# Optimization experiments

Measured on AMD Instinct MI355X. Metric: run time of the kernel, lower is better.

## Reference

```python
import jax, jax.numpy as jnp
import numpy as np

D_MODEL = 1024
NUM_HEADS = 16
HEAD_DIM = D_MODEL // NUM_HEADS
THETA = 10000.0


def _rope(x, cos, sin):
    # x: [B, H, S, hd]; cos/sin: [S, hd//2] (broadcast over B, H)
    x_even = x[..., 0::2]
    x_odd = x[..., 1::2]
    y_even = x_even * cos - x_odd * sin
    y_odd = x_even * sin + x_odd * cos
    # interleave back: stack on last dim then flatten
    y = jnp.stack((y_even, y_odd), axis=-1)
    return y.reshape(x.shape)


def setup_inputs() -> dict:
    key = jax.random.key(0)
    ks = jax.random.split(key, 5)
    B, S = 2, 2048
    x = jax.random.normal(ks[0], (B, S, D_MODEL), dtype=jnp.float32)
    scale = 1.0 / np.sqrt(D_MODEL)
    Wq = jax.random.normal(ks[1], (D_MODEL, D_MODEL), dtype=jnp.float32) * scale
    Wk = jax.random.normal(ks[2], (D_MODEL, D_MODEL), dtype=jnp.float32) * scale
    Wv = jax.random.normal(ks[3], (D_MODEL, D_MODEL), dtype=jnp.float32) * scale
    Wo = jax.random.normal(ks[4], (D_MODEL, D_MODEL), dtype=jnp.float32) * scale
    token_positions = jnp.arange(S, dtype=jnp.int64 if jax.config.jax_enable_x64 else jnp.int32)
    return {"x": x, "token_positions": token_positions, "Wq": Wq, "Wk": Wk, "Wv": Wv, "Wo": Wo}


def reference(x, token_positions, Wq, Wk, Wv, Wo):
    B, S, _ = x.shape
    # nn.Linear(d,d,bias=False): y = x @ W.T
    q = (x @ Wq.T).reshape(B, S, NUM_HEADS, HEAD_DIM).transpose(0, 2, 1, 3)
    k = (x @ Wk.T).reshape(B, S, NUM_HEADS, HEAD_DIM).transpose(0, 2, 1, 3)
    v = (x @ Wv.T).reshape(B, S, NUM_HEADS, HEAD_DIM).transpose(0, 2, 1, 3)

    # RoPE tables gathered at token_positions
    freqs = 1.0 / THETA ** (jnp.arange(0, HEAD_DIM, 2, dtype=jnp.float32) / HEAD_DIM)
    angles = token_positions.astype(jnp.float32)[:, None] * freqs[None, :]  # [S, hd//2]
    cos, sin = jnp.cos(angles), jnp.sin(angles)
    q = _rope(q, cos, sin)
    k = _rope(k, cos, sin)

    scores = jnp.einsum("bhqd,bhkd->bhqk", q, k) / np.sqrt(HEAD_DIM)
    causal = jnp.tril(jnp.ones((S, S), dtype=bool))
    scores = jnp.where(causal, scores, jnp.finfo(scores.dtype).min)
    attn = jax.nn.softmax(scores, axis=-1)
    out = jnp.einsum("bhqk,bhkd->bhqd", attn, v)  # [B,H,S,hd]
    out = out.transpose(0, 2, 1, 3).reshape(B, S, D_MODEL)
    return out @ Wo.T
```

## Files before the change

### kernel.cpp

```cpp
#include <hip/hip_runtime.h>

#define S_LEN 2048
#define NH 16
#define HD 64
#define DM 1024
#define MTOT 4096

#define QSCALE 0.18033688011112042f

typedef short bf16x8 __attribute__((ext_vector_type(8)));
typedef float f32x4 __attribute__((ext_vector_type(4)));
typedef unsigned short u16x8 __attribute__((ext_vector_type(8)));

__device__ __forceinline__ unsigned short f2bf(float f) {
  unsigned int u = __builtin_bit_cast(unsigned int, f);
  u += 0x7fffu + ((u >> 16) & 1u);
  return (unsigned short)(u >> 16);
}
__device__ __forceinline__ unsigned short f2bf_fast(float f) {
  unsigned int u = __builtin_bit_cast(unsigned int, f);
  return (unsigned short)((u + 0x8000u) >> 16);
}

__device__ __forceinline__ void async_copy16(const void* g, void* l) {
  __builtin_amdgcn_global_load_lds(
      (const __attribute__((address_space(1))) unsigned int*)g,
      (__attribute__((address_space(3))) unsigned int*)l, 16, 0, 0);
}

__global__ void cvt_bf16_kernel(const float* __restrict__ src,
                                unsigned short* __restrict__ dst, int n) {
  int i = (blockIdx.x * 256 + threadIdx.x) * 8;
  if (i >= n) return;
  const float4* s = (const float4*)(src + i);
  float4 v0 = s[0], v1 = s[1];
  u16x8 o;
  o[0] = f2bf(v0.x); o[1] = f2bf(v0.y); o[2] = f2bf(v0.z); o[3] = f2bf(v0.w);
  o[4] = f2bf(v1.x); o[5] = f2bf(v1.y); o[6] = f2bf(v1.z); o[7] = f2bf(v1.w);
  *(u16x8*)(dst + i) = o;
}

__global__ void cvt_w_kernel(const float* __restrict__ w0, const float* __restrict__ w1,
                             const float* __restrict__ w2, const float* __restrict__ w3,
                             unsigned short* __restrict__ dst) {
  int z = blockIdx.y;
  const float* src = (z == 0) ? w0 : (z == 1) ? w1 : (z == 2) ? w2 : w3;
  int i = (blockIdx.x * 256 + threadIdx.x) * 8;
  const float4* s = (const float4*)(src + i);
  float4 v0 = s[0], v1 = s[1];
  u16x8 o;
  o[0] = f2bf(v0.x); o[1] = f2bf(v0.y); o[2] = f2bf(v0.z); o[3] = f2bf(v0.w);
  o[4] = f2bf(v1.x); o[5] = f2bf(v1.y); o[6] = f2bf(v1.z); o[7] = f2bf(v1.w);
  *(u16x8*)(dst + (size_t)z * DM * DM + i) = o;
}

__global__ void sincos_tab_kernel(const int* __restrict__ pos, float2* __restrict__ tab) {
  int idx = blockIdx.x * 256 + threadIdx.x;
  int s = idx >> 5, i = idx & 31;
  float fr = expf(-(float)i * 0.28782313662425574f);
  float ang = (float)pos[s] * fr;
  float sn, cs;
  sincosf(ang, &sn, &cs);
  tab[idx] = make_float2(cs, sn);
}

__device__ __forceinline__ void gemm_core(const unsigned short* __restrict__ A,
                                          const unsigned short* __restrict__ Bt,
                                          int m0, int n0, int K,
                                          unsigned short* a_lds, unsigned short* b_lds,
                                          f32x4 (&acc)[4][4]) {
  const int tid = threadIdx.x;
  const int w = tid >> 6, l = tid & 63;
  const int wr = w >> 1, wc = w & 1;
  const int c = l & 15, g = l >> 4;

  const unsigned short* gA = A + (size_t)(m0 + w * 32 + (l >> 2)) * (size_t)K + (l & 3) * 8;
  const unsigned short* gB = Bt + (size_t)(n0 + w * 32 + (l >> 2)) * (size_t)K + (l & 3) * 8;
  unsigned short* la0 = a_lds + (w * 32) * 32 + l * 8;
  unsigned short* la1 = a_lds + (w * 32 + 16) * 32 + l * 8;
  unsigned short* lb0 = b_lds + (w * 32) * 32 + l * 8;
  unsigned short* lb1 = b_lds + (w * 32 + 16) * 32 + l * 8;

  for (int kt = 0; kt < K; kt += 32) {
    async_copy16(gA + kt, la0);
    async_copy16(gA + 16 * K + kt, la1);
    async_copy16(gB + kt, lb0);
    async_copy16(gB + 16 * K + kt, lb1);
    asm volatile("s_waitcnt vmcnt(0)" ::: "memory");
    __syncthreads();
    bf16x8 af[4], bfv[4];
#pragma unroll
    for (int mi = 0; mi < 4; ++mi)
      af[mi] = *(const bf16x8*)(a_lds + (wr * 64 + mi * 16 + c) * 32 + g * 8);
#pragma unroll
    for (int ni = 0; ni < 4; ++ni)
      bfv[ni] = *(const bf16x8*)(b_lds + (wc * 64 + ni * 16 + c) * 32 + g * 8);
#pragma unroll
    for (int mi = 0; mi < 4; ++mi)
#pragma unroll
      for (int ni = 0; ni < 4; ++ni)
        acc[mi][ni] = __builtin_amdgcn_mfma_f32_16x16x32_bf16(af[mi], bfv[ni], acc[mi][ni], 0, 0, 0);
    __syncthreads();
  }
}

__global__ __launch_bounds__(256)
void gemm_qkv_kernel(const unsigned short* __restrict__ X,
                     const unsigned short* __restrict__ Wq,
                     const unsigned short* __restrict__ Wk,
                     const unsigned short* __restrict__ Wv,
                     const float2* __restrict__ tab,
                     unsigned short* __restrict__ Qb,
                     unsigned short* __restrict__ Kb,
                     unsigned short* __restrict__ Vt) {
  __shared__ unsigned short a_lds[128 * 32];
  __shared__ unsigned short b_lds[128 * 32];
  const int z = blockIdx.z;
  const unsigned short* Bt = (z == 0) ? Wq : (z == 1) ? Wk : Wv;
  const int m0 = blockIdx.x * 128, n0 = blockIdx.y * 128;

  f32x4 acc[4][4] = {};
  gemm_core(X, Bt, m0, n0, DM, a_lds, b_lds, acc);

  const int tid = threadIdx.x;
  const int w = tid >> 6, l = tid & 63;
  const int wr = w >> 1, wc = w & 1;
  const int c = l & 15, g = l >> 4;

  if (z == 2) {
#pragma unroll
    for (int mi = 0; mi < 4; ++mi)
#pragma unroll
      for (int ni = 0; ni < 4; ++ni)
#pragma unroll
        for (int r = 0; r < 4; ++r) {
          int row = m0 + wr * 64 + mi * 16 + 4 * g + r;
          int col = n0 + wc * 64 + ni * 16 + c;
          int b = row >> 11, s = row & 2047;
          int h = col >> 6, d = col & 63;
          Vt[((size_t)(b * NH + h) * HD + d) * S_LEN + s] = f2bf(acc[mi][ni][r]);
        }
  } else {
    unsigned short* QK = z ? Kb : Qb;
    const float oscale = z ? 1.0f : QSCALE;
#pragma unroll
    for (int mi = 0; mi < 4; ++mi)
#pragma unroll
      for (int ni = 0; ni < 4; ++ni) {
        int col = n0 + wc * 64 + ni * 16 + c;
        int fi = (col >> 1) & 31;
        float sgn = (col & 1) ? 1.0f : -1.0f;
#pragma unroll
        for (int r = 0; r < 4; ++r) {
          int row = m0 + wr * 64 + mi * 16 + 4 * g + r;
          int b = row >> 11, s = row & 2047;
          float v = acc[mi][ni][r];
          float p = __shfl_xor(v, 1);
          float2 csn = tab[(s << 5) | fi];
          float vr = (v * csn.x + sgn * p * csn.y) * oscale;
          int h = col >> 6, d = col & 63;
          QK[((size_t)(b * NH + h) * S_LEN + s) * HD + d] = f2bf(vr);
        }
      }
  }
}

__global__ __launch_bounds__(256)
void gemm_out_kernel(const unsigned short* __restrict__ A,
                     const unsigned short* __restrict__ Wo,
                     float* __restrict__ out) {
  __shared__ unsigned short a_lds[128 * 32];
  __shared__ unsigned short b_lds[128 * 32];
  const int m0 = blockIdx.x * 128, n0 = blockIdx.y * 128;
  f32x4 acc[4][4] = {};
  gemm_core(A, Wo, m0, n0, DM, a_lds, b_lds, acc);

  const int tid = threadIdx.x;
  const int w = tid >> 6, l = tid & 63;
  const int wr = w >> 1, wc = w & 1;
  const int c = l & 15, g = l >> 4;
#pragma unroll
  for (int mi = 0; mi < 4; ++mi)
#pragma unroll
    for (int ni = 0; ni < 4; ++ni)
#pragma unroll
      for (int r = 0; r < 4; ++r) {
        int row = m0 + wr * 64 + mi * 16 + 4 * g + r;
        int col = n0 + wc * 64 + ni * 16 + c;
        out[(size_t)row * DM + col] = acc[mi][ni][r];
      }
}

#define PART_STRIDE 4160
__global__ __launch_bounds__(256, 4)
void attn_kernel(const unsigned short* __restrict__ Q,
                 const unsigned short* __restrict__ Kb,
                 const unsigned short* __restrict__ Vt,
                 float* __restrict__ part) {
  __shared__ char kbuf[2][8192];
  __shared__ char vbuf[2][8192];
  __shared__ unsigned short p_lds[4][16 * 64];
  const int tid = threadIdx.x;
  const int w = tid >> 6, l = tid & 63;
  const int g = l >> 4, c = l & 15;

  const unsigned int id = blockIdx.x;
  const int bh = id & 31;
  const int p = (id >> 5) & 1;
  const int qblk = 31 - (id >> 6);
  const int q0 = qblk * 64;

  const size_t base = (size_t)bh * (S_LEN * HD);
  const char* Kc = (const char*)(Kb + base);
  const char* Vc = (const char*)(Vt + base);

  const int lr = l >> 3;
  const int jsw = ((l & 7) << 4) ^ (lr << 4);
  const int r0 = w * 8 + lr;
  const int r1 = (4 + w) * 8 + lr;
  const char* ksrc0 = Kc + r0 * 128 + jsw;
  const char* ksrc1 = Kc + r1 * 128 + jsw;
  const char* vsrc0 = Vc + r0 * 4096 + jsw;
  const char* vsrc1 = Vc + r1 * 4096 + jsw;

  bf16x8 qf0, qf1;
  {
    const unsigned short* qp = Q + base + (size_t)(q0 + w * 16 + c) * HD + g * 8;
    qf0 = *(const bf16x8*)qp;
    qf1 = *(const bf16x8*)(qp + 32);
  }
  f32x4 oacc[4] = {};
  float rsum[4] = {0.f, 0.f, 0.f, 0.f};
  unsigned short* pl = &p_lds[w][0];
  const int csw = (c & 7) << 4;

  auto stage = [&](int buf, int t) {
    char* kd = &kbuf[buf][w * 1024 + l * 16];
    char* vd = &vbuf[buf][w * 1024 + l * 16];
    size_t ko = (size_t)t * 8192;
    size_t vo = (size_t)t * 128;
    async_copy16(ksrc0 + ko, kd);
    async_copy16(ksrc1 + ko, kd + 4096);
    async_copy16(vsrc0 + vo, vd);
    async_copy16(vsrc1 + vo, vd + 4096);
  };

  stage(0, p);
  asm volatile("s_waitcnt vmcnt(0)" ::: "memory");
  __syncthreads();
  int cur = 0;

  for (int t = p; t <= qblk; t += 2) {
    if (t + 2 <= qblk) stage(cur ^ 1, t + 2);
    const char* kl = kbuf[cur];
    const char* vl = vbuf[cur];
    const int kv0 = t * 64;

    f32x4 sc[4] = {};
    __builtin_amdgcn_s_setprio(1);
#pragma unroll
    for (int nt = 0; nt < 4; ++nt) {
      bf16x8 k0 = *(const bf16x8*)(kl + (nt * 16 + c) * 128 + ((g * 16) ^ csw));
      bf16x8 k1 = *(const bf16x8*)(kl + (nt * 16 + c) * 128 + ((64 + g * 16) ^ csw));
      sc[nt] = __builtin_amdgcn_mfma_f32_16x16x32_bf16(qf0, k0, sc[nt], 0, 0, 0);
      sc[nt] = __builtin_amdgcn_mfma_f32_16x16x32_bf16(qf1, k1, sc[nt], 0, 0, 0);
    }
    __builtin_amdgcn_s_setprio(0);

    if (t == qblk) {
#pragma unroll
      for (int nt = 0; nt < 4; ++nt)
#pragma unroll
        for (int r = 0; r < 4; ++r) {
          int kvi = kv0 + nt * 16 + c;
          int qi = q0 + w * 16 + 4 * g + r;
          sc[nt][r] = exp2f((kvi > qi) ? -1e30f : sc[nt][r]);
        }
    } else {
#pragma unroll
      for (int nt = 0; nt < 4; ++nt)
#pragma unroll
        for (int r = 0; r < 4; ++r)
          sc[nt][r] = exp2f(sc[nt][r]);
    }
#pragma unroll
    for (int nt = 0; nt < 4; ++nt)
#pragma unroll
      for (int r = 0; r < 4; ++r) {
        float pv = sc[nt][r];
        rsum[r] += pv;
        int row = 4 * g + r, col = nt * 16 + c;
        int byte = row * 128 + ((col * 2) ^ ((row & 7) << 4));
        *(unsigned short*)((char*)pl + byte) = f2bf_fast(pv);
      }
    asm volatile("" ::: "memory");
    __builtin_amdgcn_s_setprio(1);
#pragma unroll
    for (int ks = 0; ks < 2; ++ks) {
      int pbyte = c * 128 + ((ks * 64 + g * 16) ^ csw);
      bf16x8 pf = *(const bf16x8*)((char*)pl + pbyte);
#pragma unroll
      for (int nt = 0; nt < 4; ++nt) {
        bf16x8 vf = *(const bf16x8*)(vl + (nt * 16 + c) * 128 + ((ks * 64 + g * 16) ^ csw));
        oacc[nt] = __builtin_amdgcn_mfma_f32_16x16x32_bf16(pf, vf, oacc[nt], 0, 0, 0);
      }
    }
    __builtin_amdgcn_s_setprio(0);
    asm volatile("" ::: "memory");

    asm volatile("s_waitcnt vmcnt(0)" ::: "memory");
    __syncthreads();
    cur ^= 1;
  }

#pragma unroll
  for (int r = 0; r < 4; ++r) {
    float s = rsum[r];
    s += __shfl_xor(s, 1);
    s += __shfl_xor(s, 2);
    s += __shfl_xor(s, 4);
    s += __shfl_xor(s, 8);
    rsum[r] = s;
  }
  float* pa = part + ((size_t)(bh * 32 + qblk) * 2 + p) * PART_STRIDE;
#pragma unroll
  for (int nt = 0; nt < 4; ++nt)
#pragma unroll
    for (int r = 0; r < 4; ++r) {
      int row = w * 16 + 4 * g + r;
      int col = nt * 16 + c;
      __builtin_nontemporal_store(oacc[nt][r], &pa[row * 64 + col]);
    }
  if (c == 0) {
#pragma unroll
    for (int r = 0; r < 4; ++r) {
      int row = w * 16 + 4 * g + r;
      __builtin_nontemporal_store(rsum[r], &pa[4096 + row]);
    }
  }
}

__global__ __launch_bounds__(256)
void combine_kernel(const float* __restrict__ part, unsigned short* __restrict__ Ob) {
  const int qblk = blockIdx.x & 31;
  const int bh = blockIdx.x >> 5;
  const int b = bh >> 4, h = bh & 15;
  const int tid = threadIdx.x;
  const int row = tid >> 2, colb = (tid & 3) * 16;

  const float* p0 = part + ((size_t)(bh * 32 + qblk) * 2 + 0) * PART_STRIDE;
  const float* p1 = p0 + PART_STRIDE;
  float s0 = __builtin_nontemporal_load(&p0[4096 + row]);
  float s1 = __builtin_nontemporal_load(&p1[4096 + row]);
  float inv = 1.0f / (s0 + s1);

  int token = qblk * 64 + row;
  unsigned short* dst = Ob + ((size_t)b * S_LEN + token) * DM + h * HD + colb;
  const f32x4* a0 = (const f32x4*)(p0 + row * 64 + colb);
  const f32x4* a1 = (const f32x4*)(p1 + row * 64 + colb);
  u16x8 o0, o1;
#pragma unroll
  for (int q = 0; q < 2; ++q) {
    f32x4 v0 = __builtin_nontemporal_load(&a0[2 * q]);
    f32x4 v1 = __builtin_nontemporal_load(&a1[2 * q]);
    f32x4 w0 = __builtin_nontemporal_load(&a0[2 * q + 1]);
    f32x4 w1 = __builtin_nontemporal_load(&a1[2 * q + 1]);
    u16x8& oo = q ? o1 : o0;
    oo[0] = f2bf((v0[0] + v1[0]) * inv);
    oo[1] = f2bf((v0[1] + v1[1]) * inv);
    oo[2] = f2bf((v0[2] + v1[2]) * inv);
    oo[3] = f2bf((v0[3] + v1[3]) * inv);
    oo[4] = f2bf((w0[0] + w1[0]) * inv);
    oo[5] = f2bf((w0[1] + w1[1]) * inv);
    oo[6] = f2bf((w0[2] + w1[2]) * inv);
    oo[7] = f2bf((w0[3] + w1[3]) * inv);
  }
  *(u16x8*)dst = o0;
  *(u16x8*)(dst + 8) = o1;
}

extern "C" void kernel_launch(void* const* d_in, const int* in_sizes, int n_in,
                              void* d_out, int out_size, void* d_ws, size_t ws_size,
                              hipStream_t stream) {
  const float* x = (const float*)d_in[0];
  const int* tpos = (const int*)d_in[1];
  const float* wq = (const float*)d_in[2];
  const float* wk = (const float*)d_in[3];
  const float* wv = (const float*)d_in[4];
  const float* wo = (const float*)d_in[5];
  float* out = (float*)d_out;

  char* ws = (char*)d_ws;
  unsigned short* xb = (unsigned short*)(ws);
  unsigned short* wqb = (unsigned short*)(ws + 8388608);
  unsigned short* wkb = wqb + DM * DM;
  unsigned short* wvb = wqb + 2 * DM * DM;
  unsigned short* wob = wqb + 3 * DM * DM;
  unsigned short* qb = (unsigned short*)(ws + 16777216);
  unsigned short* kb = (unsigned short*)(ws + 16777216 + 8388608);
  unsigned short* vt = (unsigned short*)(ws + 16777216 + 2 * 8388608);
  unsigned short* ab = (unsigned short*)(ws + 16777216 + 3 * 8388608);
  float2* tab = (float2*)(ws + 50331648);
  float* part = (float*)(ws + 50855936);

  cvt_bf16_kernel<<<2048, 256, 0, stream>>>(x, xb, MTOT * DM);
  cvt_w_kernel<<<dim3(512, 4), 256, 0, stream>>>(wq, wk, wv, wo, wqb);
  sincos_tab_kernel<<<256, 256, 0, stream>>>(tpos, tab);

  gemm_qkv_kernel<<<dim3(32, 8, 3), 256, 0, stream>>>(xb, wqb, wkb, wvb, tab, qb, kb, vt);
  attn_kernel<<<2048, 256, 0, stream>>>(qb, kb, vt, part);
  combine_kernel<<<1024, 256, 0, stream>>>(part, ab);
  gemm_out_kernel<<<dim3(32, 8), 256, 0, stream>>>(ab, wob, out);
}
```

Baseline: 140.5 us.

## Widen GEMM K-tile to 64 with XOR-swizzled LDS layout

The shared GEMM core now loads a 64-element (128-byte) K slice per iteration instead of 32. Each 16-byte chunk is XOR-swizzled by row so the MFMA fragment reads avoid LDS bank conflicts. This halves the number of barrier/wait iterations and doubles the MFMA work per sync. In exchange LDS use grows to 32 KB per block, which may lower occupancy.

New measurement: 134.6 us. 4.2% less time.

```diff
diff --git a/kernel.cpp b/kernel.cpp
--- a/kernel.cpp
+++ b/kernel.cpp
@@ -67,39 +67,45 @@
 __device__ __forceinline__ void gemm_core(const unsigned short* __restrict__ A,
                                           const unsigned short* __restrict__ Bt,
                                           int m0, int n0, int K,
-                                          unsigned short* a_lds, unsigned short* b_lds,
+                                          char* a_lds, char* b_lds,
                                           f32x4 (&acc)[4][4]) {
   const int tid = threadIdx.x;
   const int w = tid >> 6, l = tid & 63;
   const int wr = w >> 1, wc = w & 1;
   const int c = l & 15, g = l >> 4;
 
-  const unsigned short* gA = A + (size_t)(m0 + w * 32 + (l >> 2)) * (size_t)K + (l & 3) * 8;
-  const unsigned short* gB = Bt + (size_t)(n0 + w * 32 + (l >> 2)) * (size_t)K + (l & 3) * 8;
-  unsigned short* la0 = a_lds + (w * 32) * 32 + l * 8;
-  unsigned short* la1 = a_lds + (w * 32 + 16) * 32 + l * 8;
-  unsigned short* lb0 = b_lds + (w * 32) * 32 + l * 8;
-  unsigned short* lb1 = b_lds + (w * 32 + 16) * 32 + l * 8;
-
-  for (int kt = 0; kt < K; kt += 32) {
-    async_copy16(gA + kt, la0);
-    async_copy16(gA + 16 * K + kt, la1);
-    async_copy16(gB + kt, lb0);
-    async_copy16(gB + 16 * K + kt, lb1);
+  const size_t rs = (size_t)K * 2;
+  const int lr = l >> 3;
+  const int jsw = ((l & 7) ^ lr) << 4;
+  const char* srcA = (const char*)A + ((size_t)m0 + w * 8 + lr) * rs + jsw;
+  const char* srcB = (const char*)Bt + ((size_t)n0 + w * 8 + lr) * rs + jsw;
+  char* dstA = a_lds + w * 1024 + l * 16;
+  char* dstB = b_lds + w * 1024 + l * 16;
+  const int csw = (c & 7) << 4;
+
+  for (int kt = 0; kt < (int)rs; kt += 128) {
+#pragma unroll
+    for (int i = 0; i < 4; ++i) {
+      async_copy16(srcA + (size_t)i * 32 * rs + kt, dstA + i * 4096);
+      async_copy16(srcB + (size_t)i * 32 * rs + kt, dstB + i * 4096);
+    }
     asm volatile("s_waitcnt vmcnt(0)" ::: "memory");
     __syncthreads();
-    bf16x8 af[4], bfv[4];
-#pragma unroll
-    for (int mi = 0; mi < 4; ++mi)
-      af[mi] = *(const bf16x8*)(a_lds + (wr * 64 + mi * 16 + c) * 32 + g * 8);
-#pragma unroll
-    for (int ni = 0; ni < 4; ++ni)
-      bfv[ni] = *(const bf16x8*)(b_lds + (wc * 64 + ni * 16 + c) * 32 + g * 8);
-#pragma unroll
-    for (int mi = 0; mi < 4; ++mi)
+#pragma unroll
+    for (int kk = 0; kk < 2; ++kk) {
+      bf16x8 af[4], bfv[4];
+#pragma unroll
+      for (int mi = 0; mi < 4; ++mi)
+        af[mi] = *(const bf16x8*)(a_lds + (wr * 64 + mi * 16 + c) * 128 + ((kk * 64 + g * 16) ^ csw));
 #pragma unroll
       for (int ni = 0; ni < 4; ++ni)
-        acc[mi][ni] = __builtin_amdgcn_mfma_f32_16x16x32_bf16(af[mi], bfv[ni], acc[mi][ni], 0, 0, 0);
+        bfv[ni] = *(const bf16x8*)(b_lds + (wc * 64 + ni * 16 + c) * 128 + ((kk * 64 + g * 16) ^ csw));
+#pragma unroll
+      for (int mi = 0; mi < 4; ++mi)
+#pragma unroll
+        for (int ni = 0; ni < 4; ++ni)
+          acc[mi][ni] = __builtin_amdgcn_mfma_f32_16x16x32_bf16(af[mi], bfv[ni], acc[mi][ni], 0, 0, 0);
+    }
     __syncthreads();
   }
 }
@@ -113,8 +119,8 @@
                      unsigned short* __restrict__ Qb,
                      unsigned short* __restrict__ Kb,
                      unsigned short* __restrict__ Vt) {
-  __shared__ unsigned short a_lds[128 * 32];
-  __shared__ unsigned short b_lds[128 * 32];
+  __shared__ char a_lds[128 * 128];
+  __shared__ char b_lds[128 * 128];
   const int z = blockIdx.z;
   const unsigned short* Bt = (z == 0) ? Wq : (z == 1) ? Wk : Wv;
   const int m0 = blockIdx.x * 128, n0 = blockIdx.y * 128;
@@ -169,8 +175,8 @@
 void gemm_out_kernel(const unsigned short* __restrict__ A,
                      const unsigned short* __restrict__ Wo,
                      float* __restrict__ out) {
-  __shared__ unsigned short a_lds[128 * 32];
-  __shared__ unsigned short b_lds[128 * 32];
+  __shared__ char a_lds[128 * 128];
+  __shared__ char b_lds[128 * 128];
   const int m0 = blockIdx.x * 128, n0 = blockIdx.y * 128;
   f32x4 acc[4][4] = {};
   gemm_core(A, Wo, m0, n0, DM, a_lds, b_lds, acc);
```
